# Optimization experiments

Measured on AMD Instinct MI355X. Metric: run time of the kernel, lower is better.

## Reference

```python
import jax, jax.numpy as jnp
import numpy as np

N = 100000      # nodes
E = 1600000     # directed edges
LAT = 128
MAT = 8
OUT = 3


def setup_inputs() -> dict:
    key = jax.random.key(0)
    ks = jax.random.split(key, 5)
    z = jax.random.normal(ks[0], (N, LAT), dtype=jnp.float32)
    material_params = jax.random.normal(ks[1], (N, MAT), dtype=jnp.float32)
    edge_index = jax.random.randint(ks[2], (2, E), 0, N, dtype=jnp.int64)
    W1 = jax.random.normal(ks[3], (LAT + MAT, LAT), dtype=jnp.float32) * 0.05
    b1 = jnp.zeros((LAT,), dtype=jnp.float32)
    W2 = jax.random.normal(ks[4], (LAT, OUT), dtype=jnp.float32) * 0.05
    b2 = jnp.zeros((OUT,), dtype=jnp.float32)
    return {"z": z, "edge_index": edge_index, "material_params": material_params,
            "W1": W1, "b1": b1, "W2": W2, "b2": b2}


def _gcn_norm(edge_index, num_nodes):
    # PyG GCNConv default: add self-loops, symmetric normalization
    src, dst = edge_index[0], edge_index[1]
    loop = jnp.arange(num_nodes, dtype=src.dtype)
    row = jnp.concatenate([src, loop])  # message source
    col = jnp.concatenate([dst, loop])  # message target
    deg = jax.ops.segment_sum(jnp.ones_like(col, dtype=jnp.float32), col,
                              num_segments=num_nodes)
    dinv = jnp.where(deg > 0, jax.lax.rsqrt(deg), 0.0)
    norm = dinv[row] * dinv[col]        # [E + N]
    return row, col, norm


def _gcn_conv(x, W, b, row, col, norm, num_nodes):
    h = x @ W                                   # linear first (PyG order)
    msg = h[row] * norm[:, None]                # gather + scale
    agg = jax.ops.segment_sum(msg, col, num_segments=num_nodes)
    return agg + b


def reference(z, edge_index, material_params, W1, b1, W2, b2):
    row, col, norm = _gcn_norm(edge_index, N)
    x = jnp.concatenate([z, material_params], axis=1)     # [N, LAT+MAT]
    x = jax.nn.relu(_gcn_conv(x, W1, b1, row, col, norm, N))
    x = _gcn_conv(x, W2, b2, row, col, norm, N)           # [N, OUT]
    return x
```

## Files before the change

### kernel.cpp

```cpp
#include <hip/hip_runtime.h>

#define N_NODES 100000
#define N_EDGES 1600000
#define LAT 128
#define MAT 8
#define OUTC 3

#define NBKT 391
#define CAP  4608
#define CHUNK 4096

__device__ __forceinline__ unsigned int pack_bf16(float a, float b) {
    unsigned int ua = __float_as_uint(a);
    ua = (ua + 0x7fffu + ((ua >> 16) & 1u)) >> 16;
    unsigned int ub = __float_as_uint(b);
    ub = (ub + 0x7fffu + ((ub >> 16) & 1u)) >> 16;
    return ua | (ub << 16);
}

__global__ __launch_bounds__(256) void k_binA(const int* __restrict__ src,
                                              const int* __restrict__ dst,
                                              int* __restrict__ gcount,
                                              unsigned int* __restrict__ binned) {
    __shared__ int hist[NBKT];
    __shared__ int adj[NBKT];
    __shared__ int cur[NBKT];
    __shared__ int wsum[4];
    __shared__ unsigned int lbuf[CHUNK];
    __shared__ unsigned short lbkt[CHUNK];

    int t = threadIdx.x;
    int base = blockIdx.x * CHUNK;
    int nEdge = min(CHUNK, N_EDGES - base);

    for (int i = t; i < NBKT; i += 256) hist[i] = 0;
    __syncthreads();

    unsigned int pk[16];
    unsigned short bk[16];
#pragma unroll
    for (int j = 0; j < 16; ++j) {
        int li = j * 256 + t;
        if (li < nEdge) {
            int e = base + li;
            int d = dst[e];
            int s = src[e];
            pk[j] = ((unsigned int)s << 8) | (unsigned int)(d & 255);
            bk[j] = (unsigned short)(d >> 8);
            atomicAdd(&hist[bk[j]], 1);
        } else {
            bk[j] = 0xffffu;
        }
    }
    __syncthreads();

    int lane = t & 63, w = t >> 6;
    int i0 = 2 * t, i1 = 2 * t + 1;
    int h0 = (i0 < NBKT) ? hist[i0] : 0;
    int h1 = (i1 < NBKT) ? hist[i1] : 0;
    int ps = h0 + h1;
    int x = ps;
#pragma unroll
    for (int off = 1; off < 64; off <<= 1) {
        int y = __shfl_up(x, off, 64);
        if (lane >= off) x += y;
    }
    if (lane == 63) wsum[w] = x;
    __syncthreads();
    int woff = 0;
#pragma unroll
    for (int i = 0; i < 4; ++i)
        if (i < w) woff += wsum[i];
    int excl = woff + x - ps;
    if (i0 < NBKT) {
        int g0 = i0 * CAP + atomicAdd(&gcount[i0], h0);
        adj[i0] = g0 - excl;
        cur[i0] = excl;
    }
    if (i1 < NBKT) {
        int g1r = i1 * CAP + atomicAdd(&gcount[i1], h1);
        adj[i1] = g1r - (excl + h0);
        cur[i1] = excl + h0;
    }
    __syncthreads();

#pragma unroll
    for (int j = 0; j < 16; ++j) {
        if (bk[j] != 0xffffu) {
            int pos = atomicAdd(&cur[bk[j]], 1);
            lbuf[pos] = pk[j];
            lbkt[pos] = bk[j];
        }
    }
    __syncthreads();

    for (int i = t; i < nEdge; i += 256) {
        int b = lbkt[i];
        binned[adj[b] + i] = lbuf[i];
    }
}

__global__ __launch_bounds__(256) void k_bscan(const int* __restrict__ gcount,
                                               int* __restrict__ bucketBase,
                                               int* __restrict__ rowptr) {
    __shared__ int wsum[4];
    int t = threadIdx.x;
    int lane = t & 63, w = t >> 6;
    int i0 = 2 * t, i1 = 2 * t + 1;
    int h0 = (i0 < NBKT) ? gcount[i0] : 0;
    int h1 = (i1 < NBKT) ? gcount[i1] : 0;
    int ps = h0 + h1;
    int x = ps;
#pragma unroll
    for (int off = 1; off < 64; off <<= 1) {
        int y = __shfl_up(x, off, 64);
        if (lane >= off) x += y;
    }
    if (lane == 63) wsum[w] = x;
    __syncthreads();
    int woff = 0;
#pragma unroll
    for (int i = 0; i < 4; ++i)
        if (i < w) woff += wsum[i];
    int excl = woff + x - ps;
    bucketBase[i0] = excl;
    bucketBase[i1] = excl + h0;
    if (t == 0) rowptr[N_NODES] = N_EDGES;
}

__global__ __launch_bounds__(256) void k_binB(const unsigned int* __restrict__ binned,
                                              const int* __restrict__ gcount,
                                              const int* __restrict__ bucketBase,
                                              int* __restrict__ colsrc,
                                              int* __restrict__ rowptr,
                                              float* __restrict__ dinv) {
    __shared__ unsigned int lbuf[CAP];
    __shared__ int lsrc[CAP];
    __shared__ int hist[256];
    __shared__ int cur[256];
    __shared__ int wsum[4];

    int b = blockIdx.x, t = threadIdx.x;
    int cnt = min(gcount[b], CAP);
    int gb = bucketBase[b];
    const unsigned int* bp = binned + (size_t)b * CAP;

    for (int i = t; i < cnt; i += 256) lbuf[i] = bp[i];
    hist[t] = 0;
    __syncthreads();
    for (int i = t; i < cnt; i += 256) atomicAdd(&hist[lbuf[i] & 255], 1);
    __syncthreads();

    int lane = t & 63, w = t >> 6;
    int h = hist[t];
    int x = h;
#pragma unroll
    for (int off = 1; off < 64; off <<= 1) {
        int y = __shfl_up(x, off, 64);
        if (lane >= off) x += y;
    }
    if (lane == 63) wsum[w] = x;
    __syncthreads();
    int woff = 0;
#pragma unroll
    for (int i = 0; i < 4; ++i)
        if (i < w) woff += wsum[i];
    int excl = woff + x - h;
    cur[t] = excl;

    int node = b * 256 + t;
    if (node < N_NODES) {
        rowptr[node] = gb + excl;
        dinv[node] = rsqrtf((float)h + 1.0f);
    }
    __syncthreads();

    for (int i = t; i < cnt; i += 256) {
        unsigned int p = lbuf[i];
        int pos = atomicAdd(&cur[p & 255], 1);
        lsrc[pos] = (int)(p >> 8);
    }
    __syncthreads();

    for (int i = t; i < cnt; i += 256) colsrc[gb + i] = lsrc[i];
}

__global__ __launch_bounds__(256) void k_gemm1(const float* __restrict__ z,
                                               const float* __restrict__ mat,
                                               const float* __restrict__ W1,
                                               const float* __restrict__ dinv,
                                               unsigned int* __restrict__ g1h) {
    __shared__ float w1s[(LAT + MAT) * LAT];
    for (int i = threadIdx.x; i < (LAT + MAT) * LAT; i += 256) w1s[i] = W1[i];
    __syncthreads();
    int g = threadIdx.x >> 5;
    int jq = (threadIdx.x & 31) * 4;
    int n0 = blockIdx.x * 32 + g * 4;
    float acc[4][4] = {{0.f}};
    for (int k4 = 0; k4 < 32; ++k4) {
        float w[4][4];
#pragma unroll
        for (int t = 0; t < 4; ++t)
            *(float4*)&w[t][0] = *(const float4*)&w1s[(k4 * 4 + t) * LAT + jq];
#pragma unroll
        for (int i = 0; i < 4; ++i) {
            float4 xv = *(const float4*)&z[(size_t)(n0 + i) * LAT + k4 * 4];
#pragma unroll
            for (int c = 0; c < 4; ++c)
                acc[i][c] += xv.x * w[0][c] + xv.y * w[1][c] + xv.z * w[2][c] + xv.w * w[3][c];
        }
    }
#pragma unroll
    for (int h = 0; h < 2; ++h) {
        float w[4][4];
#pragma unroll
        for (int t = 0; t < 4; ++t)
            *(float4*)&w[t][0] = *(const float4*)&w1s[(LAT + h * 4 + t) * LAT + jq];
#pragma unroll
        for (int i = 0; i < 4; ++i) {
            float4 xv = *(const float4*)&mat[(size_t)(n0 + i) * MAT + h * 4];
#pragma unroll
            for (int c = 0; c < 4; ++c)
                acc[i][c] += xv.x * w[0][c] + xv.y * w[1][c] + xv.z * w[2][c] + xv.w * w[3][c];
        }
    }
#pragma unroll
    for (int i = 0; i < 4; ++i) {
        float d = dinv[n0 + i];
        unsigned int p0 = pack_bf16(acc[i][0] * d, acc[i][1] * d);
        unsigned int p1 = pack_bf16(acc[i][2] * d, acc[i][3] * d);
        *(uint2*)&g1h[(size_t)(n0 + i) * 64 + (jq >> 1)] = make_uint2(p0, p1);
    }
}

__global__ __launch_bounds__(256) void k_gather1(const unsigned int* __restrict__ g1h,
                                                 const int* __restrict__ colsrc,
                                                 const int* __restrict__ rowptr,
                                                 const float* __restrict__ dinv,
                                                 const float* __restrict__ b1,
                                                 const float* __restrict__ W2,
                                                 float* __restrict__ g2) {
    int n = blockIdx.x * 4 + (threadIdx.x >> 6);
    int lane = threadIdx.x & 63;
    unsigned int au = g1h[(size_t)n * 64 + lane];
    float ax = __uint_as_float(au << 16);
    float ay = __uint_as_float(au & 0xffff0000u);
    int e0 = rowptr[n], eEnd = rowptr[n + 1];
    for (int e = e0; e < eEnd; e += 16) {
        unsigned int u[16];
#pragma unroll
        for (int j = 0; j < 16; ++j) {
            int idx = e + j;
            bool valid = idx < eEnd;
            int cs = colsrc[valid ? idx : e0];
            int s = valid ? cs : n;
            u[j] = g1h[(size_t)s * 64 + lane];
            if (!valid) u[j] = 0;
        }
#pragma unroll
        for (int j = 0; j < 16; ++j) {
            ax += __uint_as_float(u[j] << 16);
            ay += __uint_as_float(u[j] & 0xffff0000u);
        }
    }
    float d = dinv[n];
    float2 bb = ((const float2*)b1)[lane];
    float x0 = fmaxf(ax * d + bb.x, 0.f);
    float x1 = fmaxf(ay * d + bb.y, 0.f);
    float p0 = x0 * W2[(2 * lane) * OUTC + 0] + x1 * W2[(2 * lane + 1) * OUTC + 0];
    float p1 = x0 * W2[(2 * lane) * OUTC + 1] + x1 * W2[(2 * lane + 1) * OUTC + 1];
    float p2 = x0 * W2[(2 * lane) * OUTC + 2] + x1 * W2[(2 * lane + 1) * OUTC + 2];
#pragma unroll
    for (int off = 32; off > 0; off >>= 1) {
        p0 += __shfl_down(p0, off, 64);
        p1 += __shfl_down(p1, off, 64);
        p2 += __shfl_down(p2, off, 64);
    }
    if (lane == 0) ((float4*)g2)[n] = make_float4(p0 * d, p1 * d, p2 * d, 0.f);
}

__global__ void k_gather2(const float* __restrict__ g2, const int* __restrict__ colsrc,
                          const int* __restrict__ rowptr, const float* __restrict__ dinv,
                          const float* __restrict__ b2, float* __restrict__ out) {
    int n = blockIdx.x * blockDim.x + threadIdx.x;
    if (n >= N_NODES) return;
    const float4* gv = (const float4*)g2;
    float4 a = gv[n];
    float s0 = a.x, s1 = a.y, s2 = a.z;
    int eEnd = rowptr[n + 1];
    for (int e = rowptr[n]; e < eEnd; ++e) {
        float4 v = gv[colsrc[e]];
        s0 += v.x; s1 += v.y; s2 += v.z;
    }
    float d = dinv[n];
    out[(size_t)n * 3 + 0] = s0 * d + b2[0];
    out[(size_t)n * 3 + 1] = s1 * d + b2[1];
    out[(size_t)n * 3 + 2] = s2 * d + b2[2];
}


extern "C" void kernel_launch(void* const* d_in, const int* in_sizes, int n_in,
                              void* d_out, int out_size, void* d_ws, size_t ws_size,
                              hipStream_t stream) {
    const float* z   = (const float*)d_in[0];
    const int*   ei  = (const int*)d_in[1];
    const float* mat = (const float*)d_in[2];
    const float* W1  = (const float*)d_in[3];
    const float* b1  = (const float*)d_in[4];
    const float* W2  = (const float*)d_in[5];
    const float* b2  = (const float*)d_in[6];
    float* out = (float*)d_out;

    const int* srcA = ei;
    const int* dstA = ei + N_EDGES;

    char* ws = (char*)d_ws;
    auto alloc = [&](size_t bytes) {
        char* p = ws;
        ws += (bytes + 255) & ~(size_t)255;
        return p;
    };
    int*   gcount     = (int*)alloc(512 * 4);
    int*   bucketBase = (int*)alloc(512 * 4);
    int*   rowptr     = (int*)alloc((size_t)(N_NODES + 1) * 4);
    float* dinv       = (float*)alloc((size_t)N_NODES * 4);
    int*   colsrc     = (int*)alloc((size_t)N_EDGES * 4);
    unsigned int* g1h = (unsigned int*)alloc((size_t)N_NODES * 64 * 4);
    float* g2         = (float*)alloc((size_t)N_NODES * 4 * 4);
    unsigned int* binned = g1h;

    hipMemsetAsync(gcount, 0, 512 * 4, stream);
    int nBlocksA = (N_EDGES + CHUNK - 1) / CHUNK;
    k_binA<<<nBlocksA, 256, 0, stream>>>(srcA, dstA, gcount, binned);
    k_bscan<<<1, 256, 0, stream>>>(gcount, bucketBase, rowptr);
    k_binB<<<NBKT, 256, 0, stream>>>(binned, gcount, bucketBase, colsrc, rowptr, dinv);
    k_gemm1<<<N_NODES / 32, 256, 0, stream>>>(z, mat, W1, dinv, g1h);
    k_gather1<<<N_NODES / 4, 256, 0, stream>>>(g1h, colsrc, rowptr, dinv, b1, W2, g2);
    k_gather2<<<(N_NODES + 255) / 256, 256, 0, stream>>>(g2, colsrc, rowptr, dinv, b2, out);
}
```

Baseline: 208.9 us.

## Replace FP32 FMA GEMM1 with split-bf16 MFMA persistent kernel

```diff
diff --git a/kernel.cpp b/kernel.cpp
--- a/kernel.cpp
+++ b/kernel.cpp
@@ -10,12 +10,19 @@
 #define CAP  4608
 #define CHUNK 4096
 
+typedef __attribute__((ext_vector_type(8))) short bf16x8;
+typedef __attribute__((ext_vector_type(4))) float f32x4;
+
+__device__ __forceinline__ unsigned short bf16r(float f) {
+    unsigned int u = __float_as_uint(f);
+    u = (u + 0x7fffu + ((u >> 16) & 1u)) >> 16;
+    return (unsigned short)u;
+}
+__device__ __forceinline__ float bf16f(unsigned short h) {
+    return __uint_as_float((unsigned int)h << 16);
+}
 __device__ __forceinline__ unsigned int pack_bf16(float a, float b) {
-    unsigned int ua = __float_as_uint(a);
-    ua = (ua + 0x7fffu + ((ua >> 16) & 1u)) >> 16;
-    unsigned int ub = __float_as_uint(b);
-    ub = (ub + 0x7fffu + ((ub >> 16) & 1u)) >> 16;
-    return ua | (ub << 16);
+    return (unsigned int)bf16r(a) | ((unsigned int)bf16r(b) << 16);
 }
 
 __global__ __launch_bounds__(256) void k_binA(const int* __restrict__ src,
@@ -185,51 +192,86 @@
     for (int i = t; i < cnt; i += 256) colsrc[gb + i] = lsrc[i];
 }
 
-__global__ __launch_bounds__(256) void k_gemm1(const float* __restrict__ z,
-                                               const float* __restrict__ mat,
-                                               const float* __restrict__ W1,
-                                               const float* __restrict__ dinv,
-                                               unsigned int* __restrict__ g1h) {
-    __shared__ float w1s[(LAT + MAT) * LAT];
-    for (int i = threadIdx.x; i < (LAT + MAT) * LAT; i += 256) w1s[i] = W1[i];
-    __syncthreads();
-    int g = threadIdx.x >> 5;
-    int jq = (threadIdx.x & 31) * 4;
-    int n0 = blockIdx.x * 32 + g * 4;
-    float acc[4][4] = {{0.f}};
-    for (int k4 = 0; k4 < 32; ++k4) {
-        float w[4][4];
-#pragma unroll
-        for (int t = 0; t < 4; ++t)
-            *(float4*)&w[t][0] = *(const float4*)&w1s[(k4 * 4 + t) * LAT + jq];
-#pragma unroll
-        for (int i = 0; i < 4; ++i) {
-            float4 xv = *(const float4*)&z[(size_t)(n0 + i) * LAT + k4 * 4];
-#pragma unroll
-            for (int c = 0; c < 4; ++c)
-                acc[i][c] += xv.x * w[0][c] + xv.y * w[1][c] + xv.z * w[2][c] + xv.w * w[3][c];
-        }
-    }
-#pragma unroll
-    for (int h = 0; h < 2; ++h) {
-        float w[4][4];
-#pragma unroll
-        for (int t = 0; t < 4; ++t)
-            *(float4*)&w[t][0] = *(const float4*)&w1s[(LAT + h * 4 + t) * LAT + jq];
-#pragma unroll
-        for (int i = 0; i < 4; ++i) {
-            float4 xv = *(const float4*)&mat[(size_t)(n0 + i) * MAT + h * 4];
-#pragma unroll
-            for (int c = 0; c < 4; ++c)
-                acc[i][c] += xv.x * w[0][c] + xv.y * w[1][c] + xv.z * w[2][c] + xv.w * w[3][c];
-        }
-    }
-#pragma unroll
-    for (int i = 0; i < 4; ++i) {
-        float d = dinv[n0 + i];
-        unsigned int p0 = pack_bf16(acc[i][0] * d, acc[i][1] * d);
-        unsigned int p1 = pack_bf16(acc[i][2] * d, acc[i][3] * d);
-        *(uint2*)&g1h[(size_t)(n0 + i) * 64 + (jq >> 1)] = make_uint2(p0, p1);
+__global__ void k_wsplit(const float* __restrict__ W1,
+                         unsigned short* __restrict__ w1h,
+                         unsigned short* __restrict__ w1l) {
+    int i = blockIdx.x * 256 + threadIdx.x;
+    if (i >= 160 * 128) return;
+    int k = i >> 7;
+    float w = (k < LAT + MAT) ? W1[i] : 0.f;
+    unsigned short h = bf16r(w);
+    w1h[i] = h;
+    w1l[i] = bf16r(w - bf16f(h));
+}
+
+__global__ __launch_bounds__(256) void k_gemm1m(const float* __restrict__ z,
+                                                const float* __restrict__ mat,
+                                                const unsigned short* __restrict__ w1h,
+                                                const unsigned short* __restrict__ w1l,
+                                                const float* __restrict__ dinv,
+                                                unsigned short* __restrict__ g1h) {
+    int wv = threadIdx.x >> 6;
+    int l = threadIdx.x & 63;
+    int lm = l & 15, q = l >> 4;
+
+    bf16x8 bh[2][5], bl[2][5];
+#pragma unroll
+    for (int ct = 0; ct < 2; ++ct) {
+        int col = (wv * 2 + ct) * 16 + lm;
+#pragma unroll
+        for (int ks = 0; ks < 5; ++ks) {
+#pragma unroll
+            for (int j = 0; j < 8; ++j) {
+                int k = ks * 32 + q * 8 + j;
+                bh[ct][ks][j] = (short)w1h[k * 128 + col];
+                bl[ct][ks][j] = (short)w1l[k * 128 + col];
+            }
+        }
+    }
+
+    for (int tile = blockIdx.x; tile < N_NODES / 16; tile += gridDim.x) {
+        int n0 = tile * 16;
+        int row = n0 + lm;
+        f32x4 acc0 = {0.f, 0.f, 0.f, 0.f};
+        f32x4 acc1 = {0.f, 0.f, 0.f, 0.f};
+#pragma unroll
+        for (int ks = 0; ks < 5; ++ks) {
+            float a[8];
+            if (ks < 4) {
+                float4 a0 = *(const float4*)&z[(size_t)row * LAT + ks * 32 + q * 8];
+                float4 a1 = *(const float4*)&z[(size_t)row * LAT + ks * 32 + q * 8 + 4];
+                a[0] = a0.x; a[1] = a0.y; a[2] = a0.z; a[3] = a0.w;
+                a[4] = a1.x; a[5] = a1.y; a[6] = a1.z; a[7] = a1.w;
+            } else if (q == 0) {
+                float4 m0 = *(const float4*)&mat[(size_t)row * MAT];
+                float4 m1 = *(const float4*)&mat[(size_t)row * MAT + 4];
+                a[0] = m0.x; a[1] = m0.y; a[2] = m0.z; a[3] = m0.w;
+                a[4] = m1.x; a[5] = m1.y; a[6] = m1.z; a[7] = m1.w;
+            } else {
+#pragma unroll
+                for (int j = 0; j < 8; ++j) a[j] = 0.f;
+            }
+            bf16x8 ah, al;
+#pragma unroll
+            for (int j = 0; j < 8; ++j) {
+                unsigned short h = bf16r(a[j]);
+                ah[j] = (short)h;
+                al[j] = (short)bf16r(a[j] - bf16f(h));
+            }
+            acc0 = __builtin_amdgcn_mfma_f32_16x16x32_bf16(ah, bh[0][ks], acc0, 0, 0, 0);
+            acc1 = __builtin_amdgcn_mfma_f32_16x16x32_bf16(ah, bh[1][ks], acc1, 0, 0, 0);
+            acc0 = __builtin_amdgcn_mfma_f32_16x16x32_bf16(al, bh[0][ks], acc0, 0, 0, 0);
+            acc1 = __builtin_amdgcn_mfma_f32_16x16x32_bf16(al, bh[1][ks], acc1, 0, 0, 0);
+            acc0 = __builtin_amdgcn_mfma_f32_16x16x32_bf16(ah, bl[0][ks], acc0, 0, 0, 0);
+            acc1 = __builtin_amdgcn_mfma_f32_16x16x32_bf16(ah, bl[1][ks], acc1, 0, 0, 0);
+        }
+#pragma unroll
+        for (int r = 0; r < 4; ++r) {
+            int m = q * 4 + r;
+            float d = dinv[n0 + m];
+            g1h[(size_t)(n0 + m) * 128 + (wv * 2 + 0) * 16 + lm] = bf16r(acc0[r] * d);
+            g1h[(size_t)(n0 + m) * 128 + (wv * 2 + 1) * 16 + lm] = bf16r(acc1[r] * d);
+        }
     }
 }
 
@@ -327,6 +369,8 @@
     int*   colsrc     = (int*)alloc((size_t)N_EDGES * 4);
     unsigned int* g1h = (unsigned int*)alloc((size_t)N_NODES * 64 * 4);
     float* g2         = (float*)alloc((size_t)N_NODES * 4 * 4);
+    unsigned short* w1h = (unsigned short*)alloc(160 * 128 * 2);
+    unsigned short* w1l = (unsigned short*)alloc(160 * 128 * 2);
     unsigned int* binned = g1h;
 
     hipMemsetAsync(gcount, 0, 512 * 4, stream);
@@ -334,7 +378,8 @@
     k_binA<<<nBlocksA, 256, 0, stream>>>(srcA, dstA, gcount, binned);
     k_bscan<<<1, 256, 0, stream>>>(gcount, bucketBase, rowptr);
     k_binB<<<NBKT, 256, 0, stream>>>(binned, gcount, bucketBase, colsrc, rowptr, dinv);
-    k_gemm1<<<N_NODES / 32, 256, 0, stream>>>(z, mat, W1, dinv, g1h);
+    k_wsplit<<<(160 * 128 + 255) / 256, 256, 0, stream>>>(W1, w1h, w1l);
+    k_gemm1m<<<1250, 256, 0, stream>>>(z, mat, w1h, w1l, dinv, (unsigned short*)g1h);
     k_gather1<<<N_NODES / 4, 256, 0, stream>>>(g1h, colsrc, rowptr, dinv, b1, W2, g2);
     k_gather2<<<(N_NODES + 255) / 256, 256, 0, stream>>>(g2, colsrc, rowptr, dinv, b2, out);
 }
```

After: 168.1 us. 19.5% less time.
